# Optimization experiments

Hardware: AMD Instinct MI355X
Metric: run time of the kernel (lower is better)

## Reference

```python
import jax, jax.numpy as jnp
import numpy as np

N_SRC = 100000
N_DST = 50000
N_EDGES = 1600000
D_IN = 128
D_OUT = 64


def setup_inputs() -> dict:
    key = jax.random.key(0)
    ks = jax.random.split(key, 6)
    x = jax.random.normal(ks[0], (N_SRC, D_IN), dtype=jnp.float32)
    W_l = jax.random.normal(ks[1], (D_IN, D_OUT), dtype=jnp.float32) * (1.0 / np.sqrt(D_IN))
    b_l = jax.random.normal(ks[2], (D_OUT,), dtype=jnp.float32) * 0.01
    W_r = jax.random.normal(ks[3], (D_IN, D_OUT), dtype=jnp.float32) * (1.0 / np.sqrt(D_IN))
    src = jax.random.randint(ks[4], (N_EDGES,), 0, N_SRC, dtype=jnp.int64)
    dst = jax.random.randint(ks[5], (N_EDGES,), 0, N_DST, dtype=jnp.int64)
    edge_index = jnp.stack([src, dst], axis=0)
    return {"x": x, "W_l": W_l, "b_l": b_l, "W_r": W_r,
            "edge_index": edge_index, "n_dst": N_DST}


def reference(x, W_l, b_l, W_r, edge_index, n_dst):
    src, dst = edge_index[0], edge_index[1]
    # gather source features along edges: [E, D_in]
    msgs = x[src]
    # mean aggregation at destination nodes
    agg = jax.ops.segment_sum(msgs, dst, num_segments=n_dst)          # [n_dst, D_in]
    cnt = jax.ops.segment_sum(jnp.ones_like(dst, dtype=x.dtype), dst,
                              num_segments=n_dst)                     # [n_dst]
    mean = agg / jnp.maximum(cnt, 1.0)[:, None]
    x_target = x[:n_dst]
    # SAGEConv: lin_l(mean_agg) + lin_r(x_target)
    out = mean @ W_l + b_l + x_target @ W_r                           # [n_dst, D_out]
    return jax.nn.log_softmax(out, axis=-1)
```

## Files before the change

### kernel.cpp

```cpp
#include <hip/hip_runtime.h>
#include <math.h>

#define DIN  128
#define DOUT 64
#define PROWS 64
#define XPITCH 132
#define BSH  8
#define BMSK 255
#define BCAP 8960

__device__ inline unsigned short f2bf(float f) {
    unsigned u = __float_as_uint(f);
    u += 0x7fffu + ((u >> 16) & 1u);
    return (unsigned short)(u >> 16);
}
__device__ inline float bflo(unsigned u) { return __uint_as_float(u << 16); }
__device__ inline float bfhi(unsigned u) { return __uint_as_float(u & 0xffff0000u); }

__global__ void __launch_bounds__(256) fill_k(
    const int* __restrict__ ei, unsigned* __restrict__ gTail,
    int* __restrict__ bucketBuf, int E, int nB)
{
    __shared__ int lcnt[256];
    __shared__ int lpos[256];
    __shared__ int s_gb[256];
    const int t = threadIdx.x;
    const int myb = (blockIdx.x * 256 + t) * 8;
    if (myb >= E) return;
    const bool full = (myb + 8 <= E);
    int4 sa, sb4, da, db;
    if (full) {
        sa  = *(const int4*)(ei + myb);
        sb4 = *(const int4*)(ei + myb + 4);
        da  = *(const int4*)(ei + E + myb);
        db  = *(const int4*)(ei + E + myb + 4);
    }
    lcnt[t] = 0; lpos[t] = 0;
    __syncthreads();
    if (full) {
        atomicAdd(&lcnt[da.x >> BSH], 1); atomicAdd(&lcnt[da.y >> BSH], 1);
        atomicAdd(&lcnt[da.z >> BSH], 1); atomicAdd(&lcnt[da.w >> BSH], 1);
        atomicAdd(&lcnt[db.x >> BSH], 1); atomicAdd(&lcnt[db.y >> BSH], 1);
        atomicAdd(&lcnt[db.z >> BSH], 1); atomicAdd(&lcnt[db.w >> BSH], 1);
    } else {
        for (int i = myb; i < E && i < myb + 8; ++i)
            atomicAdd(&lcnt[ei[E + i] >> BSH], 1);
    }
    __syncthreads();
    if (t < nB) s_gb[t] = (int)atomicAdd(&gTail[t], (unsigned)lcnt[t]);
    __syncthreads();
#define PLACE(S, D) { int bk = (D) >> BSH; int p = atomicAdd(&lpos[bk], 1);          \
                      unsigned pos = (unsigned)(s_gb[bk] + p);                        \
                      if (pos < BCAP) bucketBuf[(size_t)bk * BCAP + pos] =            \
                          ((S) << BSH) | ((D) & BMSK); }
    if (full) {
        PLACE(sa.x,  da.x) PLACE(sa.y,  da.y) PLACE(sa.z,  da.z) PLACE(sa.w,  da.w)
        PLACE(sb4.x, db.x) PLACE(sb4.y, db.y) PLACE(sb4.z, db.z) PLACE(sb4.w, db.w)
    } else {
        for (int i = myb; i < E && i < myb + 8; ++i) {
            int s = ei[i], d = ei[E + i];
            PLACE(s, d)
        }
    }
#undef PLACE
}

__global__ void __launch_bounds__(256) proj_k(
    const float* __restrict__ x, const float* __restrict__ Wl,
    const float* __restrict__ bl, const float* __restrict__ Wr,
    unsigned short* __restrict__ y, float* __restrict__ zout,
    int nyb, int n_src, int n_dst)
{
    __shared__ float s_x[PROWS * XPITCH];
    const int pb = blockIdx.x;
    const int t  = threadIdx.x;
    const bool isY = (pb < nyb);
    const int rowBase = (isY ? pb : pb - nyb) * PROWS;
    const int nRows = isY ? n_src : n_dst;
    const float* __restrict__ W = isY ? Wl : Wr;

    {
        const float* xsrc = x + (size_t)rowBase * DIN;
        #pragma unroll
        for (int j = 0; j < 8; ++j) {
            int fi  = t + 256 * j;
            int row = fi >> 5, c4 = fi & 31;
            if (rowBase + row < nRows) {
                float4 v = *(const float4*)(xsrc + (size_t)fi * 4);
                *(float4*)(&s_x[row * XPITCH + c4 * 4]) = v;
            }
        }
    }
    __syncthreads();

    const int cg = t & 15;
    const int rg = t >> 4;
    const int r0 = rg * 4;
    const float* wp = W + cg * 4;

    float4 acc0 = {0.f,0.f,0.f,0.f};
    float4 acc1 = {0.f,0.f,0.f,0.f};
    float4 acc2 = {0.f,0.f,0.f,0.f};
    float4 acc3 = {0.f,0.f,0.f,0.f};

#define ROWFMA(acc, xv)                                                                     \
    acc.x = fmaf(xv.w, w3.x, fmaf(xv.z, w2.x, fmaf(xv.y, w1.x, fmaf(xv.x, w0.x, acc.x)))); \
    acc.y = fmaf(xv.w, w3.y, fmaf(xv.z, w2.y, fmaf(xv.y, w1.y, fmaf(xv.x, w0.y, acc.y)))); \
    acc.z = fmaf(xv.w, w3.z, fmaf(xv.z, w2.z, fmaf(xv.y, w1.z, fmaf(xv.x, w0.z, acc.z)))); \
    acc.w = fmaf(xv.w, w3.w, fmaf(xv.z, w2.w, fmaf(xv.y, w1.w, fmaf(xv.x, w0.w, acc.w))));

    #pragma unroll 2
    for (int k = 0; k < DIN; k += 4) {
        float4 w0 = *(const float4*)(wp + (size_t)(k + 0) * DOUT);
        float4 w1 = *(const float4*)(wp + (size_t)(k + 1) * DOUT);
        float4 w2 = *(const float4*)(wp + (size_t)(k + 2) * DOUT);
        float4 w3 = *(const float4*)(wp + (size_t)(k + 3) * DOUT);
        float4 x0 = *(const float4*)(&s_x[(r0 + 0) * XPITCH + k]);
        float4 x1 = *(const float4*)(&s_x[(r0 + 1) * XPITCH + k]);
        float4 x2 = *(const float4*)(&s_x[(r0 + 2) * XPITCH + k]);
        float4 x3 = *(const float4*)(&s_x[(r0 + 3) * XPITCH + k]);
        ROWFMA(acc0, x0)
        ROWFMA(acc1, x1)
        ROWFMA(acc2, x2)
        ROWFMA(acc3, x3)
    }
#undef ROWFMA

    if (isY) {
        float4 av[4] = {acc0, acc1, acc2, acc3};
        #pragma unroll
        for (int r = 0; r < 4; ++r) {
            int row = rowBase + r0 + r;
            if (row < nRows) {
                uint2 pk;
                pk.x = (unsigned)f2bf(av[r].x) | ((unsigned)f2bf(av[r].y) << 16);
                pk.y = (unsigned)f2bf(av[r].z) | ((unsigned)f2bf(av[r].w) << 16);
                *(uint2*)(y + (size_t)row * DOUT + cg * 4) = pk;
            }
        }
    } else {
        const float4 bv = *(const float4*)(bl + cg * 4);
        float4 av[4] = {acc0, acc1, acc2, acc3};
        #pragma unroll
        for (int r = 0; r < 4; ++r) {
            int row = rowBase + r0 + r;
            if (row < nRows) {
                float4 o;
                o.x = av[r].x + bv.x; o.y = av[r].y + bv.y;
                o.z = av[r].z + bv.z; o.w = av[r].w + bv.w;
                *(float4*)(zout + (size_t)row * DOUT + cg * 4) = o;
            }
        }
    }
}

__global__ void __launch_bounds__(512) bucket_k(
    const unsigned* __restrict__ gTail, const int* __restrict__ bucketBuf,
    int* __restrict__ rs, int* __restrict__ csr, int n_dst, int nB)
{
    __shared__ int s_ent[BCAP];
    __shared__ int s_hist[256];
    __shared__ int s_ofs[256];
    __shared__ int s_part[64];
    __shared__ int s_tails[256];
    __shared__ int s_bstart;
    const int b = blockIdx.x, t = threadIdx.x;
    const int lane = t & 63, wave = t >> 6;

    if (t < 256) {
        s_tails[t] = (t < nB) ? (int)gTail[t] : 0;
        s_hist[t] = 0;
    }
    __syncthreads();
    if (t == 0) {
        int acc = 0;
        for (int j = 0; j < b; ++j) {
            int v = s_tails[j];
            acc += (v < BCAP) ? v : BCAP;
        }
        s_bstart = acc;
    }
    int m = s_tails[b]; if (m > BCAP) m = BCAP;
    __syncthreads();

    const int* bb = bucketBuf + (size_t)b * BCAP;
    const int4* bb4 = (const int4*)bb;
    int4* se4 = (int4*)s_ent;
    const int m4 = m >> 2;
    for (int i4 = t; i4 < m4; i4 += 512) {
        int4 e4 = bb4[i4];
        se4[i4] = e4;
        atomicAdd(&s_hist[e4.x & BMSK], 1);
        atomicAdd(&s_hist[e4.y & BMSK], 1);
        atomicAdd(&s_hist[e4.z & BMSK], 1);
        atomicAdd(&s_hist[e4.w & BMSK], 1);
    }
    for (int i = (m4 << 2) + t; i < m; i += 512) {
        int e = bb[i];
        s_ent[i] = e;
        atomicAdd(&s_hist[e & BMSK], 1);
    }
    __syncthreads();

    if (t < 64) {
        s_part[t] = s_hist[4*t] + s_hist[4*t+1] + s_hist[4*t+2] + s_hist[4*t+3];
    }
    __syncthreads();
    if (wave == 0) {
        int v = s_part[lane];
        for (int o = 1; o < 64; o <<= 1) {
            int u = __shfl_up(v, o);
            if (lane >= o) v += u;
        }
        s_part[lane] = v;
    }
    __syncthreads();
    if (t < 64) {
        int base = (t == 0) ? 0 : s_part[t-1];
        int h0 = s_hist[4*t], h1 = s_hist[4*t+1], h2 = s_hist[4*t+2];
        s_ofs[4*t]   = base;
        s_ofs[4*t+1] = base + h0;
        s_ofs[4*t+2] = base + h0 + h1;
        s_ofs[4*t+3] = base + h0 + h1 + h2;
    }
    __syncthreads();

    const int dbase = b << BSH;
    int nloc = n_dst - dbase; if (nloc > 256) nloc = 256;
    const int bstart = s_bstart;
    if (t < nloc) rs[dbase + t] = bstart + s_ofs[t];
    if (t == 0)   rs[dbase + nloc] = bstart + m;
    __syncthreads();

    for (int i4 = t; i4 < m4; i4 += 512) {
        int4 e4 = se4[i4];
        int p0 = atomicAdd(&s_ofs[e4.x & BMSK], 1); csr[bstart + p0] = e4.x >> BSH;
        int p1 = atomicAdd(&s_ofs[e4.y & BMSK], 1); csr[bstart + p1] = e4.y >> BSH;
        int p2 = atomicAdd(&s_ofs[e4.z & BMSK], 1); csr[bstart + p2] = e4.z >> BSH;
        int p3 = atomicAdd(&s_ofs[e4.w & BMSK], 1); csr[bstart + p3] = e4.w >> BSH;
    }
    for (int i = (m4 << 2) + t; i < m; i += 512) {
        int e = s_ent[i];
        int p = atomicAdd(&s_ofs[e & BMSK], 1);
        csr[bstart + p] = e >> BSH;
    }
}

__global__ void __launch_bounds__(256) gather_k(
    const unsigned short* __restrict__ y,
    const int* __restrict__ rs, const int* __restrict__ csr,
    float* __restrict__ out, int n_dst)
{
    const int wave = threadIdx.x >> 6, lane = threadIdx.x & 63;
    const int row = blockIdx.x * 4 + wave;
    if (row >= n_dst) return;

    const int start = rs[row];
    const int deg = rs[row + 1] - start;
    const int g  = lane >> 3;
    const int c8 = lane & 7;
    const uint4* yw = (const uint4*)y;

    const float4 zv0 = *(const float4*)(out + (size_t)row * DOUT + c8 * 8);
    const float4 zv1 = *(const float4*)(out + (size_t)row * DOUT + c8 * 8 + 4);

    float4 a0l = {0,0,0,0}, a0h = {0,0,0,0};
    float4 a1l = {0,0,0,0}, a1h = {0,0,0,0};
    float4 a2l = {0,0,0,0}, a2h = {0,0,0,0};
    float4 a3l = {0,0,0,0}, a3h = {0,0,0,0};
    const int* srow = csr + start;

#define ACC8(al, ah, u)                                              \
    al.x += bflo(u.x); al.y += bfhi(u.x);                            \
    al.z += bflo(u.y); al.w += bfhi(u.y);                            \
    ah.x += bflo(u.z); ah.y += bfhi(u.z);                            \
    ah.z += bflo(u.w); ah.w += bfhi(u.w);

    for (int co = 0; co < deg; co += 64) {
        int rem = deg - co; if (rem > 64) rem = 64;
        int idx = (lane < rem) ? srow[co + lane] : 0;
        int i = 0;
        for (; i + 32 <= rem; i += 32) {
            int s0 = __shfl(idx, i + g);
            int s1 = __shfl(idx, i + 8 + g);
            int s2 = __shfl(idx, i + 16 + g);
            int s3 = __shfl(idx, i + 24 + g);
            uint4 u0 = yw[(size_t)s0 * 8 + c8];
            uint4 u1 = yw[(size_t)s1 * 8 + c8];
            uint4 u2 = yw[(size_t)s2 * 8 + c8];
            uint4 u3 = yw[(size_t)s3 * 8 + c8];
            ACC8(a0l, a0h, u0)
            ACC8(a1l, a1h, u1)
            ACC8(a2l, a2h, u2)
            ACC8(a3l, a3h, u3)
        }
        for (; i < rem; i += 8) {
            int e = i + g;
            int s0 = __shfl(idx, e);
            if (e < rem) {
                uint4 u = yw[(size_t)s0 * 8 + c8];
                ACC8(a0l, a0h, u)
            }
        }
    }
#undef ACC8

    float4 sl, sh;
    sl.x = (a0l.x + a1l.x) + (a2l.x + a3l.x);
    sl.y = (a0l.y + a1l.y) + (a2l.y + a3l.y);
    sl.z = (a0l.z + a1l.z) + (a2l.z + a3l.z);
    sl.w = (a0l.w + a1l.w) + (a2l.w + a3l.w);
    sh.x = (a0h.x + a1h.x) + (a2h.x + a3h.x);
    sh.y = (a0h.y + a1h.y) + (a2h.y + a3h.y);
    sh.z = (a0h.z + a1h.z) + (a2h.z + a3h.z);
    sh.w = (a0h.w + a1h.w) + (a2h.w + a3h.w);

    #pragma unroll
    for (int o = 32; o >= 8; o >>= 1) {
        sl.x += __shfl_xor(sl.x, o); sl.y += __shfl_xor(sl.y, o);
        sl.z += __shfl_xor(sl.z, o); sl.w += __shfl_xor(sl.w, o);
        sh.x += __shfl_xor(sh.x, o); sh.y += __shfl_xor(sh.y, o);
        sh.z += __shfl_xor(sh.z, o); sh.w += __shfl_xor(sh.w, o);
    }

    const float scale = 1.0f / (float)(deg > 0 ? deg : 1);
    float4 v0, v1;
    v0.x = sl.x * scale + zv0.x; v0.y = sl.y * scale + zv0.y;
    v0.z = sl.z * scale + zv0.z; v0.w = sl.w * scale + zv0.w;
    v1.x = sh.x * scale + zv1.x; v1.y = sh.y * scale + zv1.y;
    v1.z = sh.z * scale + zv1.z; v1.w = sh.w * scale + zv1.w;

    float m = fmaxf(fmaxf(fmaxf(v0.x, v0.y), fmaxf(v0.z, v0.w)),
                    fmaxf(fmaxf(v1.x, v1.y), fmaxf(v1.z, v1.w)));
    for (int o = 4; o >= 1; o >>= 1) m = fmaxf(m, __shfl_xor(m, o));
    float s = expf(v0.x - m) + expf(v0.y - m) + expf(v0.z - m) + expf(v0.w - m)
            + expf(v1.x - m) + expf(v1.y - m) + expf(v1.z - m) + expf(v1.w - m);
    for (int o = 4; o >= 1; o >>= 1) s += __shfl_xor(s, o);
    const float lse = m + logf(s);

    if (lane < 8) {
        float4 o0, o1;
        o0.x = v0.x - lse; o0.y = v0.y - lse; o0.z = v0.z - lse; o0.w = v0.w - lse;
        o1.x = v1.x - lse; o1.y = v1.y - lse; o1.z = v1.z - lse; o1.w = v1.w - lse;
        *(float4*)(out + (size_t)row * DOUT + c8 * 8)     = o0;
        *(float4*)(out + (size_t)row * DOUT + c8 * 8 + 4) = o1;
    }
}

extern "C" void kernel_launch(void* const* d_in, const int* in_sizes, int n_in,
                              void* d_out, int out_size, void* d_ws, size_t ws_size,
                              hipStream_t stream)
{
    const float* x  = (const float*)d_in[0];
    const float* Wl = (const float*)d_in[1];
    const float* bl = (const float*)d_in[2];
    const float* Wr = (const float*)d_in[3];
    const int*   ei = (const int*)d_in[4];

    const int E     = in_sizes[4] / 2;
    const int n_src = in_sizes[0] / DIN;
    const int n_dst = out_size / DOUT;
    const int nB    = (n_dst + (1 << BSH) - 1) >> BSH;

    unsigned* gTail = (unsigned*)d_ws;
    int* rs  = (int*)d_ws + 256;
    int* csr = rs + (n_dst + 64);
    int* bucketBuf = csr + E;
    unsigned short* yb = (unsigned short*)(bucketBuf + (size_t)nB * BCAP);

    hipMemsetAsync(gTail, 0, 256 * sizeof(unsigned), stream);

    int nFill = (E + 2047) / 2048;
    int nyb = (n_src + PROWS - 1) / PROWS;
    int nzb = (n_dst + PROWS - 1) / PROWS;

    fill_k<<<nFill, 256, 0, stream>>>(ei, gTail, bucketBuf, E, nB);

    proj_k<<<nyb + nzb, 256, 0, stream>>>(x, Wl, bl, Wr, yb, (float*)d_out,
                                          nyb, n_src, n_dst);

    bucket_k<<<nB, 512, 0, stream>>>(gTail, bucketBuf, rs, csr, n_dst, nB);

    int gG = (n_dst + 3) / 4;
    gather_k<<<gG, 256, 0, stream>>>(yb, rs, csr, (float*)d_out, n_dst);
}
```

Measured before the change: 231.3 us.

## Fuse bucket CSR build into projection kernel with interleaved block roles

Merges the per-bucket CSR construction kernel into the projection kernel. Every P-th block does one bucket's histogram, scan and scatter, and the remaining blocks do the projection GEMM. This removes one launch and lets the latency-bound bucket work overlap with the compute-bound projection. In exchange, bucket blocks now run with 256 threads instead of 512 and read the bucket entries from global memory twice instead of caching them in shared memory.

```diff
diff --git a/kernel.cpp b/kernel.cpp
--- a/kernel.cpp
+++ b/kernel.cpp
@@ -65,15 +65,104 @@
 #undef PLACE
 }
 
-__global__ void __launch_bounds__(256) proj_k(
+__global__ void __launch_bounds__(256) pb_k(
+    const unsigned* __restrict__ gTail, const int* __restrict__ bucketBuf,
+    int* __restrict__ rs, int* __restrict__ csr,
     const float* __restrict__ x, const float* __restrict__ Wl,
     const float* __restrict__ bl, const float* __restrict__ Wr,
     unsigned short* __restrict__ y, float* __restrict__ zout,
-    int nyb, int n_src, int n_dst)
+    int nyb, int n_src, int n_dst, int nB, int P)
 {
     __shared__ float s_x[PROWS * XPITCH];
-    const int pb = blockIdx.x;
-    const int t  = threadIdx.x;
+    const int b = blockIdx.x;
+    const int fq = b / P;
+    const bool isB = ((b % P) == 0) && (fq < nB);
+    const int t = threadIdx.x;
+
+    if (isB) {
+        int* s_i    = (int*)s_x;
+        int* s_hist = s_i;
+        int* s_ofs  = s_i + 256;
+        int* s_part = s_i + 512;
+        int* s_tails= s_i + 576;
+        const int lane = t & 63, wave = t >> 6;
+
+        s_tails[t] = (t < nB) ? (int)gTail[t] : 0;
+        s_hist[t] = 0;
+        __syncthreads();
+        if (t == 0) {
+            int acc = 0;
+            for (int j = 0; j < fq; ++j) {
+                int v = s_tails[j];
+                acc += (v < BCAP) ? v : BCAP;
+            }
+            s_i[832] = acc;
+        }
+        int m = s_tails[fq]; if (m > BCAP) m = BCAP;
+        __syncthreads();
+
+        const int* bb = bucketBuf + (size_t)fq * BCAP;
+        const int4* bb4 = (const int4*)bb;
+        const int m4 = m >> 2;
+        for (int i4 = t; i4 < m4; i4 += 256) {
+            int4 e4 = bb4[i4];
+            atomicAdd(&s_hist[e4.x & BMSK], 1);
+            atomicAdd(&s_hist[e4.y & BMSK], 1);
+            atomicAdd(&s_hist[e4.z & BMSK], 1);
+            atomicAdd(&s_hist[e4.w & BMSK], 1);
+        }
+        for (int i = (m4 << 2) + t; i < m; i += 256) {
+            atomicAdd(&s_hist[bb[i] & BMSK], 1);
+        }
+        __syncthreads();
+
+        if (t < 64) {
+            s_part[t] = s_hist[4*t] + s_hist[4*t+1] + s_hist[4*t+2] + s_hist[4*t+3];
+        }
+        __syncthreads();
+        if (wave == 0) {
+            int v = s_part[lane];
+            for (int o = 1; o < 64; o <<= 1) {
+                int u = __shfl_up(v, o);
+                if (lane >= o) v += u;
+            }
+            s_part[lane] = v;
+        }
+        __syncthreads();
+        if (t < 64) {
+            int base = (t == 0) ? 0 : s_part[t-1];
+            int h0 = s_hist[4*t], h1 = s_hist[4*t+1], h2 = s_hist[4*t+2];
+            s_ofs[4*t]   = base;
+            s_ofs[4*t+1] = base + h0;
+            s_ofs[4*t+2] = base + h0 + h1;
+            s_ofs[4*t+3] = base + h0 + h1 + h2;
+        }
+        __syncthreads();
+
+        const int dbase = fq << BSH;
+        int nloc = n_dst - dbase; if (nloc > 256) nloc = 256;
+        const int bstart = s_i[832];
+        if (t < nloc) rs[dbase + t] = bstart + s_ofs[t];
+        if (t == 0)   rs[dbase + nloc] = bstart + m;
+        __syncthreads();
+
+        for (int i4 = t; i4 < m4; i4 += 256) {
+            int4 e4 = bb4[i4];
+            int p0 = atomicAdd(&s_ofs[e4.x & BMSK], 1); csr[bstart + p0] = e4.x >> BSH;
+            int p1 = atomicAdd(&s_ofs[e4.y & BMSK], 1); csr[bstart + p1] = e4.y >> BSH;
+            int p2 = atomicAdd(&s_ofs[e4.z & BMSK], 1); csr[bstart + p2] = e4.z >> BSH;
+            int p3 = atomicAdd(&s_ofs[e4.w & BMSK], 1); csr[bstart + p3] = e4.w >> BSH;
+        }
+        for (int i = (m4 << 2) + t; i < m; i += 256) {
+            int e = bb[i];
+            int p = atomicAdd(&s_ofs[e & BMSK], 1);
+            csr[bstart + p] = e >> BSH;
+        }
+        return;
+    }
+
+    const int bucketsBefore = (fq + 1 < nB) ? (fq + 1) : nB;
+    const int pb = b - bucketsBefore;
     const bool isY = (pb < nyb);
     const int rowBase = (isY ? pb : pb - nyb) * PROWS;
     const int nRows = isY ? n_src : n_dst;
@@ -151,98 +240,6 @@
                 *(float4*)(zout + (size_t)row * DOUT + cg * 4) = o;
             }
         }
-    }
-}
-
-__global__ void __launch_bounds__(512) bucket_k(
-    const unsigned* __restrict__ gTail, const int* __restrict__ bucketBuf,
-    int* __restrict__ rs, int* __restrict__ csr, int n_dst, int nB)
-{
-    __shared__ int s_ent[BCAP];
-    __shared__ int s_hist[256];
-    __shared__ int s_ofs[256];
-    __shared__ int s_part[64];
-    __shared__ int s_tails[256];
-    __shared__ int s_bstart;
-    const int b = blockIdx.x, t = threadIdx.x;
-    const int lane = t & 63, wave = t >> 6;
-
-    if (t < 256) {
-        s_tails[t] = (t < nB) ? (int)gTail[t] : 0;
-        s_hist[t] = 0;
-    }
-    __syncthreads();
-    if (t == 0) {
-        int acc = 0;
-        for (int j = 0; j < b; ++j) {
-            int v = s_tails[j];
-            acc += (v < BCAP) ? v : BCAP;
-        }
-        s_bstart = acc;
-    }
-    int m = s_tails[b]; if (m > BCAP) m = BCAP;
-    __syncthreads();
-
-    const int* bb = bucketBuf + (size_t)b * BCAP;
-    const int4* bb4 = (const int4*)bb;
-    int4* se4 = (int4*)s_ent;
-    const int m4 = m >> 2;
-    for (int i4 = t; i4 < m4; i4 += 512) {
-        int4 e4 = bb4[i4];
-        se4[i4] = e4;
-        atomicAdd(&s_hist[e4.x & BMSK], 1);
-        atomicAdd(&s_hist[e4.y & BMSK], 1);
-        atomicAdd(&s_hist[e4.z & BMSK], 1);
-        atomicAdd(&s_hist[e4.w & BMSK], 1);
-    }
-    for (int i = (m4 << 2) + t; i < m; i += 512) {
-        int e = bb[i];
-        s_ent[i] = e;
-        atomicAdd(&s_hist[e & BMSK], 1);
-    }
-    __syncthreads();
-
-    if (t < 64) {
-        s_part[t] = s_hist[4*t] + s_hist[4*t+1] + s_hist[4*t+2] + s_hist[4*t+3];
-    }
-    __syncthreads();
-    if (wave == 0) {
-        int v = s_part[lane];
-        for (int o = 1; o < 64; o <<= 1) {
-            int u = __shfl_up(v, o);
-            if (lane >= o) v += u;
-        }
-        s_part[lane] = v;
-    }
-    __syncthreads();
-    if (t < 64) {
-        int base = (t == 0) ? 0 : s_part[t-1];
-        int h0 = s_hist[4*t], h1 = s_hist[4*t+1], h2 = s_hist[4*t+2];
-        s_ofs[4*t]   = base;
-        s_ofs[4*t+1] = base + h0;
-        s_ofs[4*t+2] = base + h0 + h1;
-        s_ofs[4*t+3] = base + h0 + h1 + h2;
-    }
-    __syncthreads();
-
-    const int dbase = b << BSH;
-    int nloc = n_dst - dbase; if (nloc > 256) nloc = 256;
-    const int bstart = s_bstart;
-    if (t < nloc) rs[dbase + t] = bstart + s_ofs[t];
-    if (t == 0)   rs[dbase + nloc] = bstart + m;
-    __syncthreads();
-
-    for (int i4 = t; i4 < m4; i4 += 512) {
-        int4 e4 = se4[i4];
-        int p0 = atomicAdd(&s_ofs[e4.x & BMSK], 1); csr[bstart + p0] = e4.x >> BSH;
-        int p1 = atomicAdd(&s_ofs[e4.y & BMSK], 1); csr[bstart + p1] = e4.y >> BSH;
-        int p2 = atomicAdd(&s_ofs[e4.z & BMSK], 1); csr[bstart + p2] = e4.z >> BSH;
-        int p3 = atomicAdd(&s_ofs[e4.w & BMSK], 1); csr[bstart + p3] = e4.w >> BSH;
-    }
-    for (int i = (m4 << 2) + t; i < m; i += 512) {
-        int e = s_ent[i];
-        int p = atomicAdd(&s_ofs[e & BMSK], 1);
-        csr[bstart + p] = e >> BSH;
     }
 }
 
@@ -373,13 +370,15 @@
     int nFill = (E + 2047) / 2048;
     int nyb = (n_src + PROWS - 1) / PROWS;
     int nzb = (n_dst + PROWS - 1) / PROWS;
+    int nProj = nyb + nzb;
+    int totalPB = nProj + nB;
+    int P = (totalPB + nB - 1) / nB;
 
     fill_k<<<nFill, 256, 0, stream>>>(ei, gTail, bucketBuf, E, nB);
 
-    proj_k<<<nyb + nzb, 256, 0, stream>>>(x, Wl, bl, Wr, yb, (float*)d_out,
-                                          nyb, n_src, n_dst);
-
-    bucket_k<<<nB, 512, 0, stream>>>(gTail, bucketBuf, rs, csr, n_dst, nB);
+    pb_k<<<totalPB, 256, 0, stream>>>(
+        gTail, bucketBuf, rs, csr, x, Wl, bl, Wr, yb, (float*)d_out,
+        nyb, n_src, n_dst, nB, P);
 
     int gG = (n_dst + 3) / 4;
     gather_k<<<gG, 256, 0, stream>>>(yb, rs, csr, (float*)d_out, n_dst);
```

Measured after the change: 223.6 us. -3.3%, faster.
